# Kernel optimization log

Measured on AMD Instinct MI355X. Metric: run time of the kernel, lower is better.

## Reference

```python
import jax, jax.numpy as jnp
import numpy as np

D_MODEL = 1024
NUM_HEADS = 16
D_K = D_MODEL // NUM_HEADS
ALPHA = 1.0
BANDWIDTH = 1.0
A_EXP = 0.5
DIST_SCALE = float(D_K)  # is_rescale_dist=True, alpha<2 -> d_k
D_INTRINSIC = D_K        # alpha<2 branch
EPS = 1e-12              # F.normalize eps


def setup_inputs() -> dict:
    key = jax.random.key(0)
    ks = jax.random.split(key, 8)
    B, S = 4, 2048
    s = 1.0 / np.sqrt(D_MODEL)
    return {
        "queries": jax.random.normal(ks[0], (B, S, D_MODEL), jnp.float32),
        "keys": jax.random.normal(ks[1], (B, S, D_MODEL), jnp.float32),
        "values": jax.random.normal(ks[2], (B, S, D_MODEL), jnp.float32),
        "Wq": jax.random.normal(ks[3], (D_MODEL, D_MODEL), jnp.float32) * s,
        "Wk": jax.random.normal(ks[4], (D_MODEL, D_MODEL), jnp.float32) * s,
        "Wv": jax.random.normal(ks[5], (D_MODEL, D_MODEL), jnp.float32) * s,
        "Wo": jax.random.normal(ks[6], (D_MODEL, D_MODEL), jnp.float32) * s,
        "bo": jax.random.normal(ks[7], (D_MODEL,), jnp.float32) * 0.02,
    }


def _split_heads(x):
    B, S, _ = x.shape
    return x.reshape(B, S, NUM_HEADS, D_K).transpose(0, 2, 1, 3)  # [B,H,S,d_k]


def reference(queries, keys, values, Wq, Wk, Wv, Wo, bo):
    q = _split_heads(queries @ Wq.T)
    k = _split_heads(keys @ Wk.T)
    v = _split_heads(values @ Wv.T)

    # torch.cdist(q, k, p=2): pairwise Euclidean distance  [B,H,S,S]
    q2 = jnp.sum(q * q, axis=-1)  # [B,H,S]
    k2 = jnp.sum(k * k, axis=-1)  # [B,H,S]
    qk = jnp.einsum("bhsd,bhtd->bhst", q, k)
    g_dist = jnp.sqrt(jnp.maximum(q2[..., :, None] + k2[..., None, :] - 2.0 * qk, 0.0))
    g_dist = g_dist / DIST_SCALE

    # alpha < 2 -> power-law kernel
    compat = (1.0 + g_dist / (BANDWIDTH ** 0.5)) ** (-(D_INTRINSIC + ALPHA))

    # a > 0 -> Sinkhorn-style dual row/col renormalization
    N_R = jnp.sum(compat, axis=-1)  # [B,H,S]
    N_C = jnp.sum(compat, axis=-2)  # [B,H,S]
    K_tilde = (N_R ** (-A_EXP))[..., :, None] * compat * (N_C ** (-A_EXP))[..., None, :]

    # F.normalize(p=1, dim=3): divide by max(L1 norm, eps); K_tilde >= 0
    value_weights = K_tilde / jnp.maximum(jnp.sum(K_tilde, axis=-1, keepdims=True), EPS)

    attn = jnp.einsum("bhst,bhtd->bhsd", value_weights, v)  # [B,H,S,d_k]
    B, H, S, _ = attn.shape
    merged = attn.transpose(0, 2, 1, 3).reshape(B, S, D_MODEL)
    return merged @ Wo.T + bo
```

## Files before the change

### kernel.cpp

```cpp
#include <hip/hip_runtime.h>

#define D_MODEL 1024
#define NHEADS  16
#define DK      64
#define S_LEN   2048
#define BATCH   4
#define BH      (BATCH * NHEADS)
#define M_ROWS  (BATCH * S_LEN)

typedef float  f32x4 __attribute__((ext_vector_type(4)));
typedef short  s16x8 __attribute__((ext_vector_type(8)));
typedef unsigned short u16;
typedef u16 us8 __attribute__((ext_vector_type(8)));

__device__ __forceinline__ u16 f2bf(float f) {
    unsigned u = __builtin_bit_cast(unsigned, f);
    u += 0x7FFFu + ((u >> 16) & 1u);
    return (u16)(u >> 16);
}
__device__ __forceinline__ float bf2f(u16 b) {
    unsigned u = ((unsigned)b) << 16;
    return __builtin_bit_cast(float, u);
}

__device__ __forceinline__ float compat_fn(float d2) {
    float g = __builtin_amdgcn_sqrtf(fmaxf(d2, 0.0f)) * 0.015625f;
    float p = 1.0f + g;
    return __builtin_amdgcn_exp2f(-65.0f * __builtin_amdgcn_logf(p));
}

__device__ __forceinline__ void gll16(const void* g, void* l) {
    __builtin_amdgcn_global_load_lds(
        (const __attribute__((address_space(1))) void*)g,
        (__attribute__((address_space(3))) void*)l, 16, 0, 0);
}

#define MFMA_BF16(a, b, c) __builtin_amdgcn_mfma_f32_16x16x32_bf16(a, b, c, 0, 0, 0)

__global__ __launch_bounds__(256) void split_bf16(const float* __restrict__ in,
                                                  u16* __restrict__ hi,
                                                  u16* __restrict__ lo, int n8) {
    int i = blockIdx.x * 256 + threadIdx.x;
    if (i >= n8) return;
    const float4* p = (const float4*)in;
    float4 a = p[i * 2], b = p[i * 2 + 1];
    float v[8] = {a.x, a.y, a.z, a.w, b.x, b.y, b.z, b.w};
    us8 h, l;
#pragma unroll
    for (int j = 0; j < 8; ++j) {
        u16 hb = f2bf(v[j]);
        h[j] = hb;
        l[j] = f2bf(v[j] - bf2f(hb));
    }
    ((us8*)hi)[i] = h;
    ((us8*)lo)[i] = l;
}

template <int MODE>
__global__ __launch_bounds__(256, 2) void proj_mfma(
    const u16* __restrict__ Ah, const u16* __restrict__ Al,
    const u16* __restrict__ Bh, const u16* __restrict__ Bl,
    const float* __restrict__ bias,
    float* __restrict__ outf, u16* __restrict__ ohi, u16* __restrict__ olo) {
    __shared__ __align__(16) u16 lds[4 * 128 * 64];
    u16* LAh = lds;
    u16* LAl = lds + 8192;
    u16* LBh = lds + 16384;
    u16* LBl = lds + 24576;

    const int tid  = threadIdx.x;
    const int wave = tid >> 6, lane = tid & 63;
    const int wm = wave >> 1, wn = wave & 1;
    const int l15 = lane & 15, lg = lane >> 4;
    const int flat = blockIdx.y * 8 + blockIdx.x;
    const int swz  = (flat & 7) * 64 + (flat >> 3);
    const int n0 = (swz & 7) * 128;
    const int m0 = (swz >> 3) * 128;

    const int srow = wave * 32 + (lane >> 3);
    const int scol = (lane & 7) * 8;

    f32x4 acc[4][4];
#pragma unroll
    for (int i = 0; i < 4; ++i)
#pragma unroll
        for (int j = 0; j < 4; ++j) acc[i][j] = (f32x4){0.f, 0.f, 0.f, 0.f};

#pragma unroll 1
    for (int k0 = 0; k0 < D_MODEL; k0 += 64) {
        __syncthreads();
#pragma unroll
        for (int q = 0; q < 4; ++q) {
            const size_t ga = (size_t)(m0 + srow + q * 8) * D_MODEL + k0 + scol;
            const size_t gb = (size_t)(n0 + srow + q * 8) * D_MODEL + k0 + scol;
            gll16(Ah + ga, LAh + wave * 2048 + q * 512);
            gll16(Al + ga, LAl + wave * 2048 + q * 512);
            gll16(Bh + gb, LBh + wave * 2048 + q * 512);
            gll16(Bl + gb, LBl + wave * 2048 + q * 512);
        }
        __syncthreads();
#pragma unroll
        for (int kc = 0; kc < 2; ++kc) {
            s16x8 ah[4], al[4];
#pragma unroll
            for (int fm = 0; fm < 4; ++fm) {
                const int r = wm * 64 + fm * 16 + l15;
                ah[fm] = *(const s16x8*)&LAh[r * 64 + kc * 32 + lg * 8];
                al[fm] = *(const s16x8*)&LAl[r * 64 + kc * 32 + lg * 8];
            }
#pragma unroll
            for (int fn = 0; fn < 4; ++fn) {
                const int r = wn * 64 + fn * 16 + l15;
                s16x8 bh = *(const s16x8*)&LBh[r * 64 + kc * 32 + lg * 8];
                s16x8 bl = *(const s16x8*)&LBl[r * 64 + kc * 32 + lg * 8];
#pragma unroll
                for (int fm = 0; fm < 4; ++fm) {
                    acc[fm][fn] = MFMA_BF16(ah[fm], bh, acc[fm][fn]);
                    acc[fm][fn] = MFMA_BF16(ah[fm], bl, acc[fm][fn]);
                    acc[fm][fn] = MFMA_BF16(al[fm], bh, acc[fm][fn]);
                }
            }
        }
    }
    __syncthreads();

    if (MODE == 0) {
        const int h = (n0 >> 6) + wn;
#pragma unroll
        for (int fm = 0; fm < 4; ++fm)
#pragma unroll
            for (int i = 0; i < 4; ++i) {
                const int m = m0 + wm * 64 + fm * 16 + lg * 4 + i;
                const int b = m >> 11, s = m & 2047;
                const size_t rb = ((size_t)((b * NHEADS + h) * S_LEN + s)) * DK;
#pragma unroll
                for (int fn = 0; fn < 4; ++fn) {
                    float v = acc[fm][fn][i];
                    u16 hb = f2bf(v);
                    u16 lb = f2bf(v - bf2f(hb));
                    ohi[rb + fn * 16 + l15] = hb;
                    olo[rb + fn * 16 + l15] = lb;
                }
            }
    } else if (MODE == 1) {
#pragma unroll
        for (int fm = 0; fm < 4; ++fm)
#pragma unroll
            for (int i = 0; i < 4; ++i) {
                const int m = m0 + wm * 64 + fm * 16 + lg * 4 + i;
#pragma unroll
                for (int fn = 0; fn < 4; ++fn) {
                    const int n = n0 + wn * 64 + fn * 16 + l15;
                    outf[(size_t)m * D_MODEL + n] = acc[fm][fn][i] + bias[n];
                }
            }
    } else {
        const int h  = (n0 >> 6) + wn;
        const int b  = m0 >> 11;
        const int bh = b * NHEADS + h;
        const int t_base = (m0 & 2047) + wm * 64;
        u16* T = lds + wave * 4096;
#pragma unroll
        for (int fm = 0; fm < 4; ++fm)
#pragma unroll
            for (int fn = 0; fn < 4; ++fn)
#pragma unroll
                for (int i = 0; i < 4; ++i)
                    T[(fn * 16 + l15) * 64 + fm * 16 + lg * 4 + i] = f2bf(acc[fm][fn][i]);
        __syncthreads();
#pragma unroll
        for (int j = 0; j < 8; ++j) {
            const int cid = j * 64 + lane;
            const int dr = cid >> 3;
            const int cc = (cid & 7) * 8;
            us8 v8 = *(const us8*)&T[dr * 64 + cc];
            *(us8*)&ohi[((size_t)(bh * DK + dr)) * S_LEN + t_base + cc] = v8;
        }
    }
}

__global__ __launch_bounds__(256) void row_norms(const u16* __restrict__ Qhi,
                                                 const u16* __restrict__ Qlo,
                                                 const u16* __restrict__ Khi,
                                                 const u16* __restrict__ Klo,
                                                 float* __restrict__ q2,
                                                 float* __restrict__ k2) {
    int wid  = blockIdx.x * 4 + (threadIdx.x >> 6);
    int lane = threadIdx.x & 63;
    const u16 *hi, *lo; float* dstp; int row;
    if (wid < BH * S_LEN) { hi = Qhi; lo = Qlo; dstp = q2; row = wid; }
    else                  { hi = Khi; lo = Klo; dstp = k2; row = wid - BH * S_LEN; }
    float v = bf2f(hi[(size_t)row * DK + lane]) + bf2f(lo[(size_t)row * DK + lane]);
    float s = v * v;
#pragma unroll
    for (int off = 32; off > 0; off >>= 1) s += __shfl_xor(s, off);
    if (lane == 0) dstp[row] = s;
}

__global__ __launch_bounds__(256, 4) void colsum_mfma(
    const u16* __restrict__ Qhi, const u16* __restrict__ Khi,
    const float* __restrict__ q2, const float* __restrict__ k2,
    float* __restrict__ CV) {
    const int tid  = threadIdx.x;
    const int wave = tid >> 6, lane = tid & 63;
    const int ws = wave >> 1, wt = wave & 1;
    const int l15 = lane & 15, lg = lane >> 4;
    const int flat = blockIdx.y * 32 + blockIdx.x;
    const int swz  = (flat & 7) * 256 + (flat >> 3);
    const int bh = swz >> 5;
    const int t0 = (swz & 31) * 64;
    const size_t base = (size_t)bh * S_LEN * DK;
    const u16* Kh = Khi + base;
    const u16* Qh = Qhi + base;
    const float* q2b = q2 + (size_t)bh * S_LEN;
    const float* k2b = k2 + (size_t)bh * S_LEN;

    s16x8 kh[2][2];
    float k2v[2];
#pragma unroll
    for (int ft = 0; ft < 2; ++ft) {
        const int tr = t0 + wt * 32 + ft * 16 + l15;
#pragma unroll
        for (int kc = 0; kc < 2; ++kc)
            kh[ft][kc] = *(const s16x8*)(Kh + (size_t)tr * DK + kc * 32 + lg * 8);
        k2v[ft] = k2b[tr];
    }

    s16x8 qh[2][2];
    auto loadQ = [&](int sb) {
#pragma unroll
        for (int fs = 0; fs < 2; ++fs) {
            const int qr = sb + fs * 16 + l15;
#pragma unroll
            for (int kc = 0; kc < 2; ++kc)
                qh[fs][kc] = *(const s16x8*)(Qh + (size_t)qr * DK + kc * 32 + lg * 8);
        }
    };
    loadQ(ws * 32);

    float colacc[2] = {0.f, 0.f};

#pragma unroll 1
    for (int s0 = 0; s0 < S_LEN; s0 += 64) {
        const int sb = s0 + ws * 32;
        float q2v[2][4];
#pragma unroll
        for (int fs = 0; fs < 2; ++fs)
#pragma unroll
            for (int i = 0; i < 4; ++i)
                q2v[fs][i] = q2b[sb + fs * 16 + lg * 4 + i];

        f32x4 acc[2][2];
#pragma unroll
        for (int fs = 0; fs < 2; ++fs)
#pragma unroll
            for (int ft = 0; ft < 2; ++ft) {
                acc[fs][ft] = (f32x4){0.f, 0.f, 0.f, 0.f};
#pragma unroll
                for (int kc = 0; kc < 2; ++kc)
                    acc[fs][ft] = MFMA_BF16(qh[fs][kc], kh[ft][kc], acc[fs][ft]);
            }
        if (s0 + 64 < S_LEN) loadQ(s0 + 64 + ws * 32);

#pragma unroll
        for (int fs = 0; fs < 2; ++fs)
#pragma unroll
            for (int ft = 0; ft < 2; ++ft)
#pragma unroll
                for (int i = 0; i < 4; ++i) {
                    float d2 = q2v[fs][i] + k2v[ft] - 2.0f * acc[fs][ft][i];
                    colacc[ft] += compat_fn(d2);
                }
    }
#pragma unroll
    for (int ft = 0; ft < 2; ++ft) {
        colacc[ft] += __shfl_xor(colacc[ft], 16);
        colacc[ft] += __shfl_xor(colacc[ft], 32);
    }
    __shared__ float cs[4][64];
    if (lg == 0) {
        cs[wave][wt * 32 + l15]      = colacc[0];
        cs[wave][wt * 32 + 16 + l15] = colacc[1];
    }
    __syncthreads();
    if (tid < 64) {
        int wtj = tid >> 5;
        float s = cs[wtj][tid] + cs[wtj + 2][tid];
        CV[(size_t)bh * S_LEN + t0 + tid] = 1.0f / __builtin_amdgcn_sqrtf(s);
    }
}

__global__ __launch_bounds__(256, 3) void attn_mfma(
    const u16* __restrict__ Qhi, const u16* __restrict__ Qlo,
    const u16* __restrict__ Khi, const u16* __restrict__ Klo,
    const u16* __restrict__ VThi,
    const float* __restrict__ q2, const float* __restrict__ k2,
    const float* __restrict__ CV,
    u16* __restrict__ ATTNhi, u16* __restrict__ ATTNlo) {
    __shared__ __align__(16) u16 Wb[2][64][72];
    __shared__ float rsum[2][64];
    const int tid  = threadIdx.x;
    const int wave = tid >> 6, lane = tid & 63;
    const int ws = wave >> 1, wt = wave & 1;
    const int l15 = lane & 15, lg = lane >> 4;
    const int flat = blockIdx.y * 32 + blockIdx.x;
    const int swz  = (flat & 7) * 256 + (flat >> 3);
    const int bh = swz >> 5;
    const int s0 = (swz & 31) * 64;
    const int b = bh >> 4, h = bh & 15;
    const size_t base = (size_t)bh * S_LEN * DK;
    const u16* Qh = Qhi + base;
    const u16* Ql = Qlo + base;
    const u16* Kh = Khi + base;
    const u16* Kl = Klo + base;
    const u16* Vh = VThi + base;
    const float* q2b = q2 + (size_t)bh * S_LEN;
    const float* k2b = k2 + (size_t)bh * S_LEN;
    const float* CVb = CV + (size_t)bh * S_LEN;

    s16x8 qh[2][2], qlr[2][2];
#pragma unroll
    for (int fs = 0; fs < 2; ++fs) {
        const int qr = s0 + ws * 32 + fs * 16 + l15;
#pragma unroll
        for (int kc = 0; kc < 2; ++kc) {
            qh[fs][kc]  = *(const s16x8*)(Qh + (size_t)qr * DK + kc * 32 + lg * 8);
            qlr[fs][kc] = *(const s16x8*)(Ql + (size_t)qr * DK + kc * 32 + lg * 8);
        }
    }
    float q2v[2][4];
#pragma unroll
    for (int fs = 0; fs < 2; ++fs)
#pragma unroll
        for (int i = 0; i < 4; ++i)
            q2v[fs][i] = q2b[s0 + ws * 32 + fs * 16 + lg * 4 + i];

    s16x8 kh[2][2], kl[2][2];
    auto loadK = [&](int tc) {
#pragma unroll
        for (int ft = 0; ft < 2; ++ft) {
            const int tr = tc + wt * 32 + ft * 16 + l15;
#pragma unroll
            for (int kc = 0; kc < 2; ++kc) {
                kh[ft][kc] = *(const s16x8*)(Kh + (size_t)tr * DK + kc * 32 + lg * 8);
                kl[ft][kc] = *(const s16x8*)(Kl + (size_t)tr * DK + kc * 32 + lg * 8);
            }
        }
    };
    loadK(0);

    f32x4 o[2][2];
#pragma unroll
    for (int fs = 0; fs < 2; ++fs)
#pragma unroll
        for (int fd = 0; fd < 2; ++fd)
            o[fs][fd] = (f32x4){0.f, 0.f, 0.f, 0.f};
    float rowacc[2][4] = {};

#pragma unroll 1
    for (int t0 = 0; t0 < S_LEN; t0 += 64) {
        const int buf = (t0 >> 6) & 1;
        s16x8 vv[2][2];
#pragma unroll
        for (int fd = 0; fd < 2; ++fd) {
            const int dr = wt * 32 + fd * 16 + l15;
#pragma unroll
            for (int kc = 0; kc < 2; ++kc)
                vv[fd][kc] = *(const s16x8*)(Vh + (size_t)dr * S_LEN + t0 + kc * 32 + lg * 8);
        }
        float k2v[2], cv2[2];
#pragma unroll
        for (int ft = 0; ft < 2; ++ft) {
            const int tr = t0 + wt * 32 + ft * 16 + l15;
            k2v[ft] = k2b[tr];
            cv2[ft] = CVb[tr];
        }

        f32x4 acc[2][2];
#pragma unroll
        for (int fs = 0; fs < 2; ++fs)
#pragma unroll
            for (int ft = 0; ft < 2; ++ft) {
                acc[fs][ft] = (f32x4){0.f, 0.f, 0.f, 0.f};
#pragma unroll
                for (int kc = 0; kc < 2; ++kc) {
                    acc[fs][ft] = MFMA_BF16(qh[fs][kc],  kh[ft][kc], acc[fs][ft]);
                    acc[fs][ft] = MFMA_BF16(qh[fs][kc],  kl[ft][kc], acc[fs][ft]);
                    acc[fs][ft] = MFMA_BF16(qlr[fs][kc], kh[ft][kc], acc[fs][ft]);
                }
            }
        if (t0 + 64 < S_LEN) loadK(t0 + 64);

#pragma unroll
        for (int fs = 0; fs < 2; ++fs)
#pragma unroll
            for (int ft = 0; ft < 2; ++ft)
#pragma unroll
                for (int i = 0; i < 4; ++i) {
                    float d2 = q2v[fs][i] + k2v[ft] - 2.0f * acc[fs][ft][i];
                    float w  = compat_fn(d2) * cv2[ft];
                    rowacc[fs][i] += w;
                    Wb[buf][ws * 32 + fs * 16 + lg * 4 + i][wt * 32 + ft * 16 + l15] = f2bf(w);
                }
        __syncthreads();

        s16x8 wh[2][2];
#pragma unroll
        for (int fs = 0; fs < 2; ++fs) {
            const int sl = ws * 32 + fs * 16 + l15;
#pragma unroll
            for (int kc = 0; kc < 2; ++kc)
                wh[fs][kc] = *(const s16x8*)&Wb[buf][sl][kc * 32 + lg * 8];
        }
#pragma unroll
        for (int fs = 0; fs < 2; ++fs)
#pragma unroll
            for (int fd = 0; fd < 2; ++fd)
#pragma unroll
                for (int kc = 0; kc < 2; ++kc)
                    o[fs][fd] = MFMA_BF16(wh[fs][kc], vv[fd][kc], o[fs][fd]);
    }

#pragma unroll
    for (int fs = 0; fs < 2; ++fs)
#pragma unroll
        for (int i = 0; i < 4; ++i) {
            float r = rowacc[fs][i];
            r += __shfl_xor(r, 1);
            r += __shfl_xor(r, 2);
            r += __shfl_xor(r, 4);
            r += __shfl_xor(r, 8);
            rowacc[fs][i] = r;
        }
    if (l15 == 0) {
#pragma unroll
        for (int fs = 0; fs < 2; ++fs)
#pragma unroll
            for (int i = 0; i < 4; ++i)
                rsum[wt][ws * 32 + fs * 16 + lg * 4 + i] = rowacc[fs][i];
    }
    __syncthreads();

#pragma unroll
    for (int fs = 0; fs < 2; ++fs)
#pragma unroll
        for (int i = 0; i < 4; ++i) {
            const int sl   = ws * 32 + fs * 16 + lg * 4 + i;
            const float inv = 1.0f / (rsum[0][sl] + rsum[1][sl]);
            const int srow = s0 + sl;
#pragma unroll
            for (int fd = 0; fd < 2; ++fd) {
                const int d = wt * 32 + fd * 16 + l15;
                float v = o[fs][fd][i] * inv;
                u16 hb = f2bf(v);
                u16 lb = f2bf(v - bf2f(hb));
                size_t idx = ((size_t)(b * S_LEN + srow)) * D_MODEL + h * DK + d;
                ATTNhi[idx] = hb;
                ATTNlo[idx] = lb;
            }
        }
}

extern "C" void kernel_launch(void* const* d_in, const int* in_sizes, int n_in,
                              void* d_out, int out_size, void* d_ws, size_t ws_size,
                              hipStream_t stream) {
    const float* queries = (const float*)d_in[0];
    const float* keys    = (const float*)d_in[1];
    const float* values  = (const float*)d_in[2];
    const float* Wq      = (const float*)d_in[3];
    const float* Wk      = (const float*)d_in[4];
    const float* Wv      = (const float*)d_in[5];
    const float* Wo      = (const float*)d_in[6];
    const float* bo      = (const float*)d_in[7];
    float* out = (float*)d_out;

    const size_t NW = (size_t)D_MODEL * D_MODEL;
    const size_t NX = (size_t)M_ROWS * D_MODEL;
    u16* base = (u16*)d_ws;
    size_t off = 0;
    auto take = [&](size_t n) { u16* r = base + off; off += n; return r; };
    u16 *Wqh = take(NW), *Wql = take(NW), *Wkh = take(NW), *Wkl = take(NW);
    u16 *Wvh = take(NW), *Wvl = take(NW), *Woh = take(NW), *Wol = take(NW);
    u16 *Xqh = take(NX), *Xql = take(NX);
    u16 *Xkh = take(NX), *Xkl = take(NX);
    u16 *Xvh = take(NX), *Xvl = take(NX);
    u16 *Qhi = take(NX), *Qlo = take(NX), *Khi = take(NX), *Klo = take(NX);
    u16 *VThi = take(NX);
    u16* ATTNhi = Xqh;
    u16* ATTNlo = Xql;
    float* q2  = (float*)Xkh;
    float* k2  = q2 + (size_t)BH * S_LEN;
    float* CVa = k2 + (size_t)BH * S_LEN;

    split_bf16<<<(int)(NX / 8 / 256), 256, 0, stream>>>(queries, Xqh, Xql, (int)(NX / 8));
    split_bf16<<<(int)(NX / 8 / 256), 256, 0, stream>>>(keys,    Xkh, Xkl, (int)(NX / 8));
    split_bf16<<<(int)(NX / 8 / 256), 256, 0, stream>>>(values,  Xvh, Xvl, (int)(NX / 8));
    split_bf16<<<(int)(NW / 8 / 256), 256, 0, stream>>>(Wq, Wqh, Wql, (int)(NW / 8));
    split_bf16<<<(int)(NW / 8 / 256), 256, 0, stream>>>(Wk, Wkh, Wkl, (int)(NW / 8));
    split_bf16<<<(int)(NW / 8 / 256), 256, 0, stream>>>(Wv, Wvh, Wvl, (int)(NW / 8));
    split_bf16<<<(int)(NW / 8 / 256), 256, 0, stream>>>(Wo, Woh, Wol, (int)(NW / 8));

    dim3 gproj(D_MODEL / 128, M_ROWS / 128);
    proj_mfma<0><<<gproj, 256, 0, stream>>>(Xqh, Xql, Wqh, Wql, nullptr, nullptr, Qhi, Qlo);
    proj_mfma<0><<<gproj, 256, 0, stream>>>(Xkh, Xkl, Wkh, Wkl, nullptr, nullptr, Khi, Klo);
    proj_mfma<2><<<gproj, 256, 0, stream>>>(Xvh, Xvl, Wvh, Wvl, nullptr, nullptr, VThi, nullptr);

    row_norms<<<(2 * BH * S_LEN) / 4, 256, 0, stream>>>(Qhi, Qlo, Khi, Klo, q2, k2);

    dim3 gpass(S_LEN / 64, BH);
    colsum_mfma<<<gpass, 256, 0, stream>>>(Qhi, Khi, q2, k2, CVa);
    attn_mfma<<<gpass, 256, 0, stream>>>(Qhi, Qlo, Khi, Klo, VThi, q2, k2, CVa, ATTNhi, ATTNlo);

    proj_mfma<1><<<gproj, 256, 0, stream>>>(ATTNhi, ATTNlo, Woh, Wol, bo, out, nullptr, nullptr);
}
```

Before: 895.8 us.

## Give each wave its own 16 query rows and drop block barriers in attention loop

Restructures the attention kernel so each wave owns 16 query rows across all 64 keys per tile, computing S^T via swapped MFMA operands. Probability weights go into a per-wave, rotation-swizzled LDS slice, which removes the per-iteration __syncthreads. K fragments are double-buffered per 16-key subtile, and the q2/k2 bias is folded into the accumulator initialisation. The trade-off is that each wave now loads all four V fragments and all K rows itself, which raises global/L2 traffic and register pressure. The final row-sum readback from LDS has no barrier and relies on intra-wave ordering.

Measured after the change: 1.265 ms. 41.2% more time.

```diff
diff --git a/kernel.cpp b/kernel.cpp
--- a/kernel.cpp
+++ b/kernel.cpp
@@ -297,11 +297,10 @@
     const float* __restrict__ q2, const float* __restrict__ k2,
     const float* __restrict__ CV,
     u16* __restrict__ ATTNhi, u16* __restrict__ ATTNlo) {
-    __shared__ __align__(16) u16 Wb[2][64][72];
-    __shared__ float rsum[2][64];
+    __shared__ __align__(16) u16 Wlds[4][16][64];
+    __shared__ float Rlds[64];
     const int tid  = threadIdx.x;
     const int wave = tid >> 6, lane = tid & 63;
-    const int ws = wave >> 1, wt = wave & 1;
     const int l15 = lane & 15, lg = lane >> 4;
     const int flat = blockIdx.y * 32 + blockIdx.x;
     const int swz  = (flat & 7) * 256 + (flat >> 3);
@@ -318,147 +317,112 @@
     const float* k2b = k2 + (size_t)bh * S_LEN;
     const float* CVb = CV + (size_t)bh * S_LEN;
 
-    s16x8 qh[2][2], qlr[2][2];
-#pragma unroll
-    for (int fs = 0; fs < 2; ++fs) {
-        const int qr = s0 + ws * 32 + fs * 16 + l15;
+    const int srow = s0 + wave * 16 + l15;
+    s16x8 qhf[2], qlf[2];
+#pragma unroll
+    for (int kc = 0; kc < 2; ++kc) {
+        qhf[kc] = *(const s16x8*)(Qh + (size_t)srow * DK + kc * 32 + lg * 8);
+        qlf[kc] = *(const s16x8*)(Ql + (size_t)srow * DK + kc * 32 + lg * 8);
+    }
+    const float q2s = q2b[srow];
+
+    char* const wrow = (char*)&Wlds[wave][l15][0];
+    const int rot = (l15 & 7) << 4;
+    const int wlg = lg * 8 + rot;
+    const int rlg = lg * 16 + rot;
+
+    struct KF { s16x8 kh[2], kl[2]; float4 k24, cv4; };
+    KF buf[2];
+    auto loadKF = [&](KF& kf, int t0, int ft) {
+        const int tr = t0 + ft * 16 + l15;
 #pragma unroll
         for (int kc = 0; kc < 2; ++kc) {
-            qh[fs][kc]  = *(const s16x8*)(Qh + (size_t)qr * DK + kc * 32 + lg * 8);
-            qlr[fs][kc] = *(const s16x8*)(Ql + (size_t)qr * DK + kc * 32 + lg * 8);
-        }
-    }
-    float q2v[2][4];
-#pragma unroll
-    for (int fs = 0; fs < 2; ++fs)
-#pragma unroll
-        for (int i = 0; i < 4; ++i)
-            q2v[fs][i] = q2b[s0 + ws * 32 + fs * 16 + lg * 4 + i];
-
-    s16x8 kh[2][2], kl[2][2];
-    auto loadK = [&](int tc) {
-#pragma unroll
-        for (int ft = 0; ft < 2; ++ft) {
-            const int tr = tc + wt * 32 + ft * 16 + l15;
-#pragma unroll
-            for (int kc = 0; kc < 2; ++kc) {
-                kh[ft][kc] = *(const s16x8*)(Kh + (size_t)tr * DK + kc * 32 + lg * 8);
-                kl[ft][kc] = *(const s16x8*)(Kl + (size_t)tr * DK + kc * 32 + lg * 8);
-            }
-        }
+            kf.kh[kc] = *(const s16x8*)(Kh + (size_t)tr * DK + kc * 32 + lg * 8);
+            kf.kl[kc] = *(const s16x8*)(Kl + (size_t)tr * DK + kc * 32 + lg * 8);
+        }
+        kf.k24 = *(const float4*)&k2b[t0 + ft * 16 + lg * 4];
+        kf.cv4 = *(const float4*)&CVb[t0 + ft * 16 + lg * 4];
     };
-    loadK(0);
-
-    f32x4 o[2][2];
-#pragma unroll
-    for (int fs = 0; fs < 2; ++fs)
-#pragma unroll
-        for (int fd = 0; fd < 2; ++fd)
-            o[fs][fd] = (f32x4){0.f, 0.f, 0.f, 0.f};
-    float rowacc[2][4] = {};
+    loadKF(buf[0], 0, 0);
+
+    f32x4 o[4];
+#pragma unroll
+    for (int fd = 0; fd < 4; ++fd) o[fd] = (f32x4){0.f, 0.f, 0.f, 0.f};
+    float rowpart = 0.f;
 
 #pragma unroll 1
     for (int t0 = 0; t0 < S_LEN; t0 += 64) {
-        const int buf = (t0 >> 6) & 1;
-        s16x8 vv[2][2];
-#pragma unroll
-        for (int fd = 0; fd < 2; ++fd) {
-            const int dr = wt * 32 + fd * 16 + l15;
+        s16x8 vv[4][2];
+#pragma unroll
+        for (int fd = 0; fd < 4; ++fd) {
+            const int dr = fd * 16 + l15;
 #pragma unroll
             for (int kc = 0; kc < 2; ++kc)
                 vv[fd][kc] = *(const s16x8*)(Vh + (size_t)dr * S_LEN + t0 + kc * 32 + lg * 8);
         }
-        float k2v[2], cv2[2];
-#pragma unroll
-        for (int ft = 0; ft < 2; ++ft) {
-            const int tr = t0 + wt * 32 + ft * 16 + l15;
-            k2v[ft] = k2b[tr];
-            cv2[ft] = CVb[tr];
-        }
-
-        f32x4 acc[2][2];
-#pragma unroll
-        for (int fs = 0; fs < 2; ++fs)
-#pragma unroll
-            for (int ft = 0; ft < 2; ++ft) {
-                acc[fs][ft] = (f32x4){0.f, 0.f, 0.f, 0.f};
-#pragma unroll
-                for (int kc = 0; kc < 2; ++kc) {
-                    acc[fs][ft] = MFMA_BF16(qh[fs][kc],  kh[ft][kc], acc[fs][ft]);
-                    acc[fs][ft] = MFMA_BF16(qh[fs][kc],  kl[ft][kc], acc[fs][ft]);
-                    acc[fs][ft] = MFMA_BF16(qlr[fs][kc], kh[ft][kc], acc[fs][ft]);
-                }
-            }
-        if (t0 + 64 < S_LEN) loadK(t0 + 64);
-
-#pragma unroll
-        for (int fs = 0; fs < 2; ++fs)
-#pragma unroll
-            for (int ft = 0; ft < 2; ++ft)
-#pragma unroll
-                for (int i = 0; i < 4; ++i) {
-                    float d2 = q2v[fs][i] + k2v[ft] - 2.0f * acc[fs][ft][i];
-                    float w  = compat_fn(d2) * cv2[ft];
-                    rowacc[fs][i] += w;
-                    Wb[buf][ws * 32 + fs * 16 + lg * 4 + i][wt * 32 + ft * 16 + l15] = f2bf(w);
-                }
-        __syncthreads();
-
-        s16x8 wh[2][2];
-#pragma unroll
-        for (int fs = 0; fs < 2; ++fs) {
-            const int sl = ws * 32 + fs * 16 + l15;
+
+#pragma unroll
+        for (int ft = 0; ft < 4; ++ft) {
+            KF& cur = buf[ft & 1];
+            {
+                int nt0 = t0, nft = ft + 1;
+                if (nft == 4) { nft = 0; nt0 += 64; }
+                if (nt0 < S_LEN) loadKF(buf[(ft & 1) ^ 1], nt0, nft);
+            }
+            f32x4 acc;
+#pragma unroll
+            for (int i = 0; i < 4; ++i) acc[i] = -0.5f * (q2s + cur.k24[i]);
+#pragma unroll
+            for (int kc = 0; kc < 2; ++kc) {
+                acc = MFMA_BF16(cur.kh[kc], qhf[kc], acc);
+                acc = MFMA_BF16(cur.kh[kc], qlf[kc], acc);
+                acc = MFMA_BF16(cur.kl[kc], qhf[kc], acc);
+            }
+            u16 wb[4];
+#pragma unroll
+            for (int i = 0; i < 4; ++i) {
+                float d2 = acc[i] * -2.0f;
+                float w  = compat_fn(d2) * cur.cv4[i];
+                rowpart += w;
+                wb[i] = f2bf(w);
+            }
+            unsigned long long pk =
+                (unsigned long long)((unsigned)wb[0] | ((unsigned)wb[1] << 16)) |
+                ((unsigned long long)((unsigned)wb[2] | ((unsigned)wb[3] << 16)) << 32);
+            *(unsigned long long*)(wrow + ((ft * 32 + wlg) & 127)) = pk;
+        }
+
+        s16x8 wf[2];
+#pragma unroll
+        for (int kc = 0; kc < 2; ++kc)
+            wf[kc] = *(const s16x8*)(wrow + ((kc * 64 + rlg) & 127));
+#pragma unroll
+        for (int fd = 0; fd < 4; ++fd)
 #pragma unroll
             for (int kc = 0; kc < 2; ++kc)
-                wh[fs][kc] = *(const s16x8*)&Wb[buf][sl][kc * 32 + lg * 8];
-        }
-#pragma unroll
-        for (int fs = 0; fs < 2; ++fs)
-#pragma unroll
-            for (int fd = 0; fd < 2; ++fd)
-#pragma unroll
-                for (int kc = 0; kc < 2; ++kc)
-                    o[fs][fd] = MFMA_BF16(wh[fs][kc], vv[fd][kc], o[fs][fd]);
-    }
-
-#pragma unroll
-    for (int fs = 0; fs < 2; ++fs)
-#pragma unroll
-        for (int i = 0; i < 4; ++i) {
-            float r = rowacc[fs][i];
-            r += __shfl_xor(r, 1);
-            r += __shfl_xor(r, 2);
-            r += __shfl_xor(r, 4);
-            r += __shfl_xor(r, 8);
-            rowacc[fs][i] = r;
-        }
-    if (l15 == 0) {
-#pragma unroll
-        for (int fs = 0; fs < 2; ++fs)
-#pragma unroll
-            for (int i = 0; i < 4; ++i)
-                rsum[wt][ws * 32 + fs * 16 + lg * 4 + i] = rowacc[fs][i];
-    }
-    __syncthreads();
-
-#pragma unroll
-    for (int fs = 0; fs < 2; ++fs)
-#pragma unroll
-        for (int i = 0; i < 4; ++i) {
-            const int sl   = ws * 32 + fs * 16 + lg * 4 + i;
-            const float inv = 1.0f / (rsum[0][sl] + rsum[1][sl]);
-            const int srow = s0 + sl;
-#pragma unroll
-            for (int fd = 0; fd < 2; ++fd) {
-                const int d = wt * 32 + fd * 16 + l15;
-                float v = o[fs][fd][i] * inv;
-                u16 hb = f2bf(v);
-                u16 lb = f2bf(v - bf2f(hb));
-                size_t idx = ((size_t)(b * S_LEN + srow)) * D_MODEL + h * DK + d;
-                ATTNhi[idx] = hb;
-                ATTNlo[idx] = lb;
-            }
-        }
+                o[fd] = MFMA_BF16(wf[kc], vv[fd][kc], o[fd]);
+    }
+
+    rowpart += __shfl_xor(rowpart, 16);
+    rowpart += __shfl_xor(rowpart, 32);
+    if (lg == 0) Rlds[wave * 16 + l15] = rowpart;
+    float4 rs4 = *(const float4*)&Rlds[wave * 16 + lg * 4];
+
+#pragma unroll
+    for (int i = 0; i < 4; ++i) {
+        const float inv = 1.0f / rs4[i];
+        const int sr = s0 + wave * 16 + lg * 4 + i;
+#pragma unroll
+        for (int fd = 0; fd < 4; ++fd) {
+            const int d = fd * 16 + l15;
+            float v = o[fd][i] * inv;
+            u16 hb = f2bf(v);
+            u16 lb = f2bf(v - bf2f(hb));
+            size_t idx = ((size_t)(b * S_LEN + sr)) * D_MODEL + h * DK + d;
+            ATTNhi[idx] = hb;
+            ATTNlo[idx] = lb;
+        }
+    }
 }
 
 extern "C" void kernel_launch(void* const* d_in, const int* in_sizes, int n_in,
```

## Software-pipeline distance MFMAs against previous tile's compat math in both kernels

Applied to the files above, without the earlier changes.

Both the column-sum kernel and the attention kernel now issue the QK MFMAs for tile i, then evaluate the power-law compat and the PV MFMA for tile i-1. The aim is to overlap MFMA latency with the transcendental and ALU work instead of waiting on results in the same iteration. The attention kernel's launch bound also rises from 3 to 4 waves-per-EU occupancy. The extra live registers for the carried accumulators and V fragments raise register pressure, and the tighter occupancy bound could cause spills.

Result: slower. 1.773 ms (+97.9%).

```diff
diff --git a/kernel.cpp b/kernel.cpp
--- a/kernel.cpp
+++ b/kernel.cpp
@@ -239,39 +239,57 @@
     loadQ(ws * 32);
 
     float colacc[2] = {0.f, 0.f};
+    f32x4 accP[2][2];
+    float4 q2P[2];
 
 #pragma unroll 1
     for (int s0 = 0; s0 < S_LEN; s0 += 64) {
         const int sb = s0 + ws * 32;
-        float q2v[2][4];
-#pragma unroll
-        for (int fs = 0; fs < 2; ++fs)
-#pragma unroll
-            for (int i = 0; i < 4; ++i)
-                q2v[fs][i] = q2b[sb + fs * 16 + lg * 4 + i];
-
-        f32x4 acc[2][2];
+        float4 q2c[2];
+#pragma unroll
+        for (int fs = 0; fs < 2; ++fs)
+            q2c[fs] = *(const float4*)&q2b[sb + fs * 16 + lg * 4];
+
+        f32x4 accC[2][2];
 #pragma unroll
         for (int fs = 0; fs < 2; ++fs)
 #pragma unroll
             for (int ft = 0; ft < 2; ++ft) {
-                acc[fs][ft] = (f32x4){0.f, 0.f, 0.f, 0.f};
+                accC[fs][ft] = (f32x4){0.f, 0.f, 0.f, 0.f};
 #pragma unroll
                 for (int kc = 0; kc < 2; ++kc)
-                    acc[fs][ft] = MFMA_BF16(qh[fs][kc], kh[ft][kc], acc[fs][ft]);
+                    accC[fs][ft] = MFMA_BF16(qh[fs][kc], kh[ft][kc], accC[fs][ft]);
             }
         if (s0 + 64 < S_LEN) loadQ(s0 + 64 + ws * 32);
 
-#pragma unroll
-        for (int fs = 0; fs < 2; ++fs)
-#pragma unroll
-            for (int ft = 0; ft < 2; ++ft)
-#pragma unroll
-                for (int i = 0; i < 4; ++i) {
-                    float d2 = q2v[fs][i] + k2v[ft] - 2.0f * acc[fs][ft][i];
-                    colacc[ft] += compat_fn(d2);
-                }
-    }
+        if (s0 > 0) {
+#pragma unroll
+            for (int fs = 0; fs < 2; ++fs)
+#pragma unroll
+                for (int ft = 0; ft < 2; ++ft)
+#pragma unroll
+                    for (int i = 0; i < 4; ++i) {
+                        float d2 = q2P[fs][i] + k2v[ft] - 2.0f * accP[fs][ft][i];
+                        colacc[ft] += compat_fn(d2);
+                    }
+        }
+#pragma unroll
+        for (int fs = 0; fs < 2; ++fs) {
+            q2P[fs] = q2c[fs];
+#pragma unroll
+            for (int ft = 0; ft < 2; ++ft) accP[fs][ft] = accC[fs][ft];
+        }
+    }
+#pragma unroll
+    for (int fs = 0; fs < 2; ++fs)
+#pragma unroll
+        for (int ft = 0; ft < 2; ++ft)
+#pragma unroll
+            for (int i = 0; i < 4; ++i) {
+                float d2 = q2P[fs][i] + k2v[ft] - 2.0f * accP[fs][ft][i];
+                colacc[ft] += compat_fn(d2);
+            }
+
 #pragma unroll
     for (int ft = 0; ft < 2; ++ft) {
         colacc[ft] += __shfl_xor(colacc[ft], 16);
@@ -290,7 +308,7 @@
     }
 }
 
-__global__ __launch_bounds__(256, 3) void attn_mfma(
+__global__ __launch_bounds__(256, 4) void attn_mfma(
     const u16* __restrict__ Qhi, const u16* __restrict__ Qlo,
     const u16* __restrict__ Khi, const u16* __restrict__ Klo,
     const u16* __restrict__ VThi,
@@ -357,9 +375,13 @@
             o[fs][fd] = (f32x4){0.f, 0.f, 0.f, 0.f};
     float rowacc[2][4] = {};
 
+    f32x4 accP[2][2];
+    s16x8 vP[2][2];
+    float k2P[2], cvP[2];
+
 #pragma unroll 1
-    for (int t0 = 0; t0 < S_LEN; t0 += 64) {
-        const int buf = (t0 >> 6) & 1;
+    for (int it = 0; it < S_LEN / 64; ++it) {
+        const int t0 = it * 64;
         s16x8 vv[2][2];
 #pragma unroll
         for (int fd = 0; fd < 2; ++fd) {
@@ -368,49 +390,94 @@
             for (int kc = 0; kc < 2; ++kc)
                 vv[fd][kc] = *(const s16x8*)(Vh + (size_t)dr * S_LEN + t0 + kc * 32 + lg * 8);
         }
-        float k2v[2], cv2[2];
+        float k2c[2], cvc[2];
 #pragma unroll
         for (int ft = 0; ft < 2; ++ft) {
             const int tr = t0 + wt * 32 + ft * 16 + l15;
-            k2v[ft] = k2b[tr];
-            cv2[ft] = CVb[tr];
-        }
-
-        f32x4 acc[2][2];
+            k2c[ft] = k2b[tr];
+            cvc[ft] = CVb[tr];
+        }
+
+        f32x4 accC[2][2];
 #pragma unroll
         for (int fs = 0; fs < 2; ++fs)
 #pragma unroll
             for (int ft = 0; ft < 2; ++ft) {
-                acc[fs][ft] = (f32x4){0.f, 0.f, 0.f, 0.f};
+                accC[fs][ft] = (f32x4){0.f, 0.f, 0.f, 0.f};
 #pragma unroll
                 for (int kc = 0; kc < 2; ++kc) {
-                    acc[fs][ft] = MFMA_BF16(qh[fs][kc],  kh[ft][kc], acc[fs][ft]);
-                    acc[fs][ft] = MFMA_BF16(qh[fs][kc],  kl[ft][kc], acc[fs][ft]);
-                    acc[fs][ft] = MFMA_BF16(qlr[fs][kc], kh[ft][kc], acc[fs][ft]);
+                    accC[fs][ft] = MFMA_BF16(qh[fs][kc],  kh[ft][kc], accC[fs][ft]);
+                    accC[fs][ft] = MFMA_BF16(qh[fs][kc],  kl[ft][kc], accC[fs][ft]);
+                    accC[fs][ft] = MFMA_BF16(qlr[fs][kc], kh[ft][kc], accC[fs][ft]);
                 }
             }
         if (t0 + 64 < S_LEN) loadK(t0 + 64);
 
+        if (it > 0) {
+            const int bufp = (it - 1) & 1;
+#pragma unroll
+            for (int fs = 0; fs < 2; ++fs)
+#pragma unroll
+                for (int ft = 0; ft < 2; ++ft)
+#pragma unroll
+                    for (int i = 0; i < 4; ++i) {
+                        float d2 = q2v[fs][i] + k2P[ft] - 2.0f * accP[fs][ft][i];
+                        float w  = compat_fn(d2) * cvP[ft];
+                        rowacc[fs][i] += w;
+                        Wb[bufp][ws * 32 + fs * 16 + lg * 4 + i][wt * 32 + ft * 16 + l15] = f2bf(w);
+                    }
+            __syncthreads();
+
+            s16x8 wh[2][2];
+#pragma unroll
+            for (int fs = 0; fs < 2; ++fs) {
+                const int sl = ws * 32 + fs * 16 + l15;
+#pragma unroll
+                for (int kc = 0; kc < 2; ++kc)
+                    wh[fs][kc] = *(const s16x8*)&Wb[bufp][sl][kc * 32 + lg * 8];
+            }
+#pragma unroll
+            for (int fs = 0; fs < 2; ++fs)
+#pragma unroll
+                for (int fd = 0; fd < 2; ++fd)
+#pragma unroll
+                    for (int kc = 0; kc < 2; ++kc)
+                        o[fs][fd] = MFMA_BF16(wh[fs][kc], vP[fd][kc], o[fs][fd]);
+        }
+
+#pragma unroll
+        for (int fs = 0; fs < 2; ++fs)
+#pragma unroll
+            for (int ft = 0; ft < 2; ++ft) accP[fs][ft] = accC[fs][ft];
+#pragma unroll
+        for (int fd = 0; fd < 2; ++fd)
+#pragma unroll
+            for (int kc = 0; kc < 2; ++kc) vP[fd][kc] = vv[fd][kc];
+#pragma unroll
+        for (int ft = 0; ft < 2; ++ft) { k2P[ft] = k2c[ft]; cvP[ft] = cvc[ft]; }
+    }
+
+    {
+        const int bufp = (S_LEN / 64 - 1) & 1;
 #pragma unroll
         for (int fs = 0; fs < 2; ++fs)
 #pragma unroll
             for (int ft = 0; ft < 2; ++ft)
 #pragma unroll
                 for (int i = 0; i < 4; ++i) {
-                    float d2 = q2v[fs][i] + k2v[ft] - 2.0f * acc[fs][ft][i];
-                    float w  = compat_fn(d2) * cv2[ft];
+                    float d2 = q2v[fs][i] + k2P[ft] - 2.0f * accP[fs][ft][i];
+                    float w  = compat_fn(d2) * cvP[ft];
                     rowacc[fs][i] += w;
-                    Wb[buf][ws * 32 + fs * 16 + lg * 4 + i][wt * 32 + ft * 16 + l15] = f2bf(w);
+                    Wb[bufp][ws * 32 + fs * 16 + lg * 4 + i][wt * 32 + ft * 16 + l15] = f2bf(w);
                 }
         __syncthreads();
-
         s16x8 wh[2][2];
 #pragma unroll
         for (int fs = 0; fs < 2; ++fs) {
             const int sl = ws * 32 + fs * 16 + l15;
 #pragma unroll
             for (int kc = 0; kc < 2; ++kc)
-                wh[fs][kc] = *(const s16x8*)&Wb[buf][sl][kc * 32 + lg * 8];
+                wh[fs][kc] = *(const s16x8*)&Wb[bufp][sl][kc * 32 + lg * 8];
         }
 #pragma unroll
         for (int fs = 0; fs < 2; ++fs)
@@ -418,7 +485,7 @@
             for (int fd = 0; fd < 2; ++fd)
 #pragma unroll
                 for (int kc = 0; kc < 2; ++kc)
-                    o[fs][fd] = MFMA_BF16(wh[fs][kc], vv[fd][kc], o[fs][fd]);
+                    o[fs][fd] = MFMA_BF16(wh[fs][kc], vP[fd][kc], o[fs][fd]);
     }
 
 #pragma unroll
```

## Transpose MFMA operands, pipeline colsum compute, pack bf16 weight stores

Applied to the files above, without the earlier changes.

Both attention kernels swap the MFMA A/B operands so each lane holds consecutive key columns for one query row. The per-key norms and column scales can then be loaded as float4, and the bf16 weights are packed with v_cvt_pk_bf16 into a single 8-byte LDS store instead of four scalar stores. The colsum kernel also software-pipelines the loop, running the compat math on the previous tile's MFMA results while the current MFMAs are in flight. attn_mfma's occupancy hint rises from 3 to 4 blocks per CU, which squeezes the register budget and could cause spills.

Measured after the change: 1.115 ms. 1.24x slower.

```diff
diff --git a/kernel.cpp b/kernel.cpp
--- a/kernel.cpp
+++ b/kernel.cpp
@@ -21,6 +21,11 @@
 __device__ __forceinline__ float bf2f(u16 b) {
     unsigned u = ((unsigned)b) << 16;
     return __builtin_bit_cast(float, u);
+}
+__device__ __forceinline__ unsigned cvt_pk_bf16(float lo, float hi) {
+    unsigned r;
+    asm("v_cvt_pk_bf16_f32 %0, %1, %2" : "=v"(r) : "v"(lo), "v"(hi));
+    return r;
 }
 
 __device__ __forceinline__ float compat_fn(float d2) {
@@ -216,14 +221,14 @@
     const float* k2b = k2 + (size_t)bh * S_LEN;
 
     s16x8 kh[2][2];
-    float k2v[2];
+    float4 k24[2];
 #pragma unroll
     for (int ft = 0; ft < 2; ++ft) {
         const int tr = t0 + wt * 32 + ft * 16 + l15;
 #pragma unroll
         for (int kc = 0; kc < 2; ++kc)
             kh[ft][kc] = *(const s16x8*)(Kh + (size_t)tr * DK + kc * 32 + lg * 8);
-        k2v[ft] = k2b[tr];
+        k24[ft] = *(const float4*)&k2b[t0 + wt * 32 + ft * 16 + lg * 4];
     }
 
     s16x8 qh[2][2];
@@ -238,49 +243,77 @@
     };
     loadQ(ws * 32);
 
-    float colacc[2] = {0.f, 0.f};
+    f32x4 colacc[2];
+    colacc[0] = (f32x4){0.f, 0.f, 0.f, 0.f};
+    colacc[1] = (f32x4){0.f, 0.f, 0.f, 0.f};
+    f32x4 accP[2][2];
+    float q2P[2];
 
 #pragma unroll 1
     for (int s0 = 0; s0 < S_LEN; s0 += 64) {
         const int sb = s0 + ws * 32;
-        float q2v[2][4];
+        float q2c[2];
+#pragma unroll
+        for (int fs = 0; fs < 2; ++fs) q2c[fs] = q2b[sb + fs * 16 + l15];
+
+        f32x4 accC[2][2];
 #pragma unroll
         for (int fs = 0; fs < 2; ++fs)
 #pragma unroll
+            for (int ft = 0; ft < 2; ++ft) {
+                accC[fs][ft] = (f32x4){0.f, 0.f, 0.f, 0.f};
+#pragma unroll
+                for (int kc = 0; kc < 2; ++kc)
+                    accC[fs][ft] = MFMA_BF16(kh[ft][kc], qh[fs][kc], accC[fs][ft]);
+            }
+        if (s0 + 64 < S_LEN) loadQ(s0 + 64 + ws * 32);
+
+        if (s0 > 0) {
+#pragma unroll
+            for (int fs = 0; fs < 2; ++fs)
+#pragma unroll
+                for (int ft = 0; ft < 2; ++ft)
+#pragma unroll
+                    for (int i = 0; i < 4; ++i) {
+                        float d2 = fmaf(-2.0f, accP[fs][ft][i], q2P[fs] + k24[ft][i]);
+                        colacc[ft][i] += compat_fn(d2);
+                    }
+        }
+#pragma unroll
+        for (int fs = 0; fs < 2; ++fs) {
+            q2P[fs] = q2c[fs];
+#pragma unroll
+            for (int ft = 0; ft < 2; ++ft) accP[fs][ft] = accC[fs][ft];
+        }
+    }
+#pragma unroll
+    for (int fs = 0; fs < 2; ++fs)
+#pragma unroll
+        for (int ft = 0; ft < 2; ++ft)
+#pragma unroll
+            for (int i = 0; i < 4; ++i) {
+                float d2 = fmaf(-2.0f, accP[fs][ft][i], q2P[fs] + k24[ft][i]);
+                colacc[ft][i] += compat_fn(d2);
+            }
+
+#pragma unroll
+    for (int ft = 0; ft < 2; ++ft)
+#pragma unroll
+        for (int i = 0; i < 4; ++i) {
+            float r = colacc[ft][i];
+            r += __shfl_xor(r, 1);
+            r += __shfl_xor(r, 2);
+            r += __shfl_xor(r, 4);
+            r += __shfl_xor(r, 8);
+            colacc[ft][i] = r;
+        }
+    __shared__ float cs[4][64];
+    if (l15 == 0) {
+#pragma unroll
+        for (int ft = 0; ft < 2; ++ft)
+#pragma unroll
             for (int i = 0; i < 4; ++i)
-                q2v[fs][i] = q2b[sb + fs * 16 + lg * 4 + i];
-
-        f32x4 acc[2][2];
-#pragma unroll
-        for (int fs = 0; fs < 2; ++fs)
-#pragma unroll
-            for (int ft = 0; ft < 2; ++ft) {
-                acc[fs][ft] = (f32x4){0.f, 0.f, 0.f, 0.f};
-#pragma unroll
-                for (int kc = 0; kc < 2; ++kc)
-                    acc[fs][ft] = MFMA_BF16(qh[fs][kc], kh[ft][kc], acc[fs][ft]);
-            }
-        if (s0 + 64 < S_LEN) loadQ(s0 + 64 + ws * 32);
-
-#pragma unroll
-        for (int fs = 0; fs < 2; ++fs)
-#pragma unroll
-            for (int ft = 0; ft < 2; ++ft)
-#pragma unroll
-                for (int i = 0; i < 4; ++i) {
-                    float d2 = q2v[fs][i] + k2v[ft] - 2.0f * acc[fs][ft][i];
-                    colacc[ft] += compat_fn(d2);
-                }
-    }
-#pragma unroll
-    for (int ft = 0; ft < 2; ++ft) {
-        colacc[ft] += __shfl_xor(colacc[ft], 16);
-        colacc[ft] += __shfl_xor(colacc[ft], 32);
-    }
-    __shared__ float cs[4][64];
-    if (lg == 0) {
-        cs[wave][wt * 32 + l15]      = colacc[0];
-        cs[wave][wt * 32 + 16 + l15] = colacc[1];
+                cs[wave][wt * 32 + ft * 16 + lg * 4 + i] = colacc[ft][i];
     }
     __syncthreads();
     if (tid < 64) {
@@ -290,7 +323,7 @@
     }
 }
 
-__global__ __launch_bounds__(256, 3) void attn_mfma(
+__global__ __launch_bounds__(256, 4) void attn_mfma(
     const u16* __restrict__ Qhi, const u16* __restrict__ Qlo,
     const u16* __restrict__ Khi, const u16* __restrict__ Klo,
     const u16* __restrict__ VThi,
@@ -319,6 +352,7 @@
     const float* CVb = CV + (size_t)bh * S_LEN;
 
     s16x8 qh[2][2], qlr[2][2];
+    float q2s[2];
 #pragma unroll
     for (int fs = 0; fs < 2; ++fs) {
         const int qr = s0 + ws * 32 + fs * 16 + l15;
@@ -327,13 +361,8 @@
             qh[fs][kc]  = *(const s16x8*)(Qh + (size_t)qr * DK + kc * 32 + lg * 8);
             qlr[fs][kc] = *(const s16x8*)(Ql + (size_t)qr * DK + kc * 32 + lg * 8);
         }
-    }
-    float q2v[2][4];
-#pragma unroll
-    for (int fs = 0; fs < 2; ++fs)
-#pragma unroll
-        for (int i = 0; i < 4; ++i)
-            q2v[fs][i] = q2b[s0 + ws * 32 + fs * 16 + lg * 4 + i];
+        q2s[fs] = q2b[qr];
+    }
 
     s16x8 kh[2][2], kl[2][2];
     auto loadK = [&](int tc) {
@@ -355,11 +384,12 @@
 #pragma unroll
         for (int fd = 0; fd < 2; ++fd)
             o[fs][fd] = (f32x4){0.f, 0.f, 0.f, 0.f};
-    float rowacc[2][4] = {};
+    float rowacc[2] = {0.f, 0.f};
 
 #pragma unroll 1
-    for (int t0 = 0; t0 < S_LEN; t0 += 64) {
-        const int buf = (t0 >> 6) & 1;
+    for (int it = 0; it < S_LEN / 64; ++it) {
+        const int t0 = it * 64;
+        const int buf = it & 1;
         s16x8 vv[2][2];
 #pragma unroll
         for (int fd = 0; fd < 2; ++fd) {
@@ -368,12 +398,12 @@
             for (int kc = 0; kc < 2; ++kc)
                 vv[fd][kc] = *(const s16x8*)(Vh + (size_t)dr * S_LEN + t0 + kc * 32 + lg * 8);
         }
-        float k2v[2], cv2[2];
+        float4 k24[2], cv4[2];
 #pragma unroll
         for (int ft = 0; ft < 2; ++ft) {
-            const int tr = t0 + wt * 32 + ft * 16 + l15;
-            k2v[ft] = k2b[tr];
-            cv2[ft] = CVb[tr];
+            const int tr4 = t0 + wt * 32 + ft * 16 + lg * 4;
+            k24[ft] = *(const float4*)&k2b[tr4];
+            cv4[ft] = *(const float4*)&CVb[tr4];
         }
 
         f32x4 acc[2][2];
@@ -384,31 +414,38 @@
                 acc[fs][ft] = (f32x4){0.f, 0.f, 0.f, 0.f};
 #pragma unroll
                 for (int kc = 0; kc < 2; ++kc) {
-                    acc[fs][ft] = MFMA_BF16(qh[fs][kc],  kh[ft][kc], acc[fs][ft]);
-                    acc[fs][ft] = MFMA_BF16(qh[fs][kc],  kl[ft][kc], acc[fs][ft]);
-                    acc[fs][ft] = MFMA_BF16(qlr[fs][kc], kh[ft][kc], acc[fs][ft]);
+                    acc[fs][ft] = MFMA_BF16(kh[ft][kc], qh[fs][kc],  acc[fs][ft]);
+                    acc[fs][ft] = MFMA_BF16(kl[ft][kc], qh[fs][kc],  acc[fs][ft]);
+                    acc[fs][ft] = MFMA_BF16(kh[ft][kc], qlr[fs][kc], acc[fs][ft]);
                 }
             }
         if (t0 + 64 < S_LEN) loadK(t0 + 64);
 
-#pragma unroll
-        for (int fs = 0; fs < 2; ++fs)
-#pragma unroll
-            for (int ft = 0; ft < 2; ++ft)
-#pragma unroll
-                for (int i = 0; i < 4; ++i) {
-                    float d2 = q2v[fs][i] + k2v[ft] - 2.0f * acc[fs][ft][i];
-                    float w  = compat_fn(d2) * cv2[ft];
-                    rowacc[fs][i] += w;
-                    Wb[buf][ws * 32 + fs * 16 + lg * 4 + i][wt * 32 + ft * 16 + l15] = f2bf(w);
-                }
-        __syncthreads();
-
-        s16x8 wh[2][2];
 #pragma unroll
         for (int fs = 0; fs < 2; ++fs) {
             const int sl = ws * 32 + fs * 16 + l15;
 #pragma unroll
+            for (int ft = 0; ft < 2; ++ft) {
+                float w[4];
+#pragma unroll
+                for (int i = 0; i < 4; ++i) {
+                    float d2 = fmaf(-2.0f, acc[fs][ft][i], q2s[fs] + k24[ft][i]);
+                    w[i] = compat_fn(d2) * cv4[ft][i];
+                    rowacc[fs] += w[i];
+                }
+                unsigned p0 = cvt_pk_bf16(w[0], w[1]);
+                unsigned p1 = cvt_pk_bf16(w[2], w[3]);
+                *(unsigned long long*)&Wb[buf][sl][wt * 32 + ft * 16 + lg * 4] =
+                    (unsigned long long)p0 | ((unsigned long long)p1 << 32);
+            }
+        }
+        __syncthreads();
+
+        s16x8 wh[2][2];
+#pragma unroll
+        for (int fs = 0; fs < 2; ++fs) {
+            const int sl = ws * 32 + fs * 16 + l15;
+#pragma unroll
             for (int kc = 0; kc < 2; ++kc)
                 wh[fs][kc] = *(const s16x8*)&Wb[buf][sl][kc * 32 + lg * 8];
         }
@@ -422,22 +459,16 @@
     }
 
 #pragma unroll
-    for (int fs = 0; fs < 2; ++fs)
-#pragma unroll
-        for (int i = 0; i < 4; ++i) {
-            float r = rowacc[fs][i];
-            r += __shfl_xor(r, 1);
-            r += __shfl_xor(r, 2);
-            r += __shfl_xor(r, 4);
-            r += __shfl_xor(r, 8);
-            rowacc[fs][i] = r;
-        }
-    if (l15 == 0) {
+    for (int fs = 0; fs < 2; ++fs) {
+        float r = rowacc[fs];
+        r += __shfl_xor(r, 16);
+        r += __shfl_xor(r, 32);
+        rowacc[fs] = r;
+    }
+    if (lg == 0) {
 #pragma unroll
         for (int fs = 0; fs < 2; ++fs)
-#pragma unroll
-            for (int i = 0; i < 4; ++i)
-                rsum[wt][ws * 32 + fs * 16 + lg * 4 + i] = rowacc[fs][i];
+            rsum[wt][ws * 32 + fs * 16 + l15] = rowacc[fs];
     }
     __syncthreads();
 
```
